# Optimization experiments

Measured on AMD Instinct MI355X. Metric: run time of the kernel, lower is better.

Reference implementation:

```python
import jax, jax.numpy as jnp
import numpy as np

N_PATCHES = 14
PS = 16            # patch size: 224 / 14
C, H_IMG, W_IMG = 3, 224, 224
HIDDEN = 768
HEADS = 12
DH = HIDDEN // HEADS
BLOCKS = 12
MLP = 4 * HIDDEN
OUT = 1000
SEQ = N_PATCHES ** 2 + 1  # 197
BATCH = 64


def get_positional_embeddings(seq_len, d):
    # sin(i/10000^(j/d)) for even j, cos(i/10000^((j-1)/d)) for odd j
    i = jnp.arange(seq_len, dtype=jnp.float32)[:, None]
    j = jnp.arange(d)[None, :]
    even = (j % 2 == 0)
    expo = jnp.where(even, j, j - 1).astype(jnp.float32) / d
    ang = i / (10000.0 ** expo)
    return jnp.where(even, jnp.sin(ang), jnp.cos(ang))


def layernorm(x, g, b, eps=1e-5):
    mu = x.mean(-1, keepdims=True)
    var = ((x - mu) ** 2).mean(-1, keepdims=True)
    return (x - mu) / jnp.sqrt(var + eps) * g + b


def mhsa(x, qw, qb, kw, kb, vw, vb):
    # x: [B,S,HIDDEN]; per-head linears qw/kw/vw: [H,DH,DH] (torch Linear weight layout)
    B, S, _ = x.shape
    xh = x.reshape(B, S, HEADS, DH)
    q = jnp.einsum('bshd,hed->bshe', xh, qw) + qb
    k = jnp.einsum('bshd,hed->bshe', xh, kw) + kb
    v = jnp.einsum('bshd,hed->bshe', xh, vw) + vb
    scores = jnp.einsum('bshe,bthe->bhst', q, k) / jnp.sqrt(jnp.float32(DH))
    attn = jax.nn.softmax(scores, axis=-1)
    out = jnp.einsum('bhst,bthe->bshe', attn, v)
    return out.reshape(B, S, HIDDEN)


def vit_block(x, p):
    ln1_g, ln1_b, qw, qb, kw, kb, vw, vb, ln2_g, ln2_b, w1, b1, w2, b2 = p
    x = x + mhsa(layernorm(x, ln1_g, ln1_b), qw, qb, kw, kb, vw, vb)
    h = layernorm(x, ln2_g, ln2_b)
    h = jax.nn.gelu(h @ w1.T + b1, approximate=False) @ w2.T + b2
    return x + h


def patchify(images):
    # [N,C,H,W] -> [N, n_patches^2, C*PS*PS], channel-major within each patch
    n = images.shape[0]
    x = images.reshape(n, C, N_PATCHES, PS, N_PATCHES, PS)
    x = x.transpose(0, 2, 4, 1, 3, 5)  # n, pi, pj, c, ps, ps
    return x.reshape(n, N_PATCHES * N_PATCHES, C * PS * PS)


def setup_inputs() -> dict:
    key = jax.random.key(0)
    ks = jax.random.split(key, 20)
    s = 0.02
    return {
        'images': jax.random.normal(ks[0], (BATCH, C, H_IMG, W_IMG), jnp.float32),
        'mapper_w': jax.random.normal(ks[1], (HIDDEN, C * PS * PS), jnp.float32) * s,
        'mapper_b': jnp.zeros((HIDDEN,), jnp.float32),
        'cls_token': jax.random.uniform(ks[2], (1, HIDDEN), jnp.float32),
        'ln1_g': jnp.ones((BLOCKS, HIDDEN), jnp.float32),
        'ln1_b': jnp.zeros((BLOCKS, HIDDEN), jnp.float32),
        'qw': jax.random.normal(ks[3], (BLOCKS, HEADS, DH, DH), jnp.float32) * s,
        'qb': jnp.zeros((BLOCKS, HEADS, DH), jnp.float32),
        'kw': jax.random.normal(ks[4], (BLOCKS, HEADS, DH, DH), jnp.float32) * s,
        'kb': jnp.zeros((BLOCKS, HEADS, DH), jnp.float32),
        'vw': jax.random.normal(ks[5], (BLOCKS, HEADS, DH, DH), jnp.float32) * s,
        'vb': jnp.zeros((BLOCKS, HEADS, DH), jnp.float32),
        'ln2_g': jnp.ones((BLOCKS, HIDDEN), jnp.float32),
        'ln2_b': jnp.zeros((BLOCKS, HIDDEN), jnp.float32),
        'w1': jax.random.normal(ks[6], (BLOCKS, MLP, HIDDEN), jnp.float32) * s,
        'b1': jnp.zeros((BLOCKS, MLP), jnp.float32),
        'w2': jax.random.normal(ks[7], (BLOCKS, HIDDEN, MLP), jnp.float32) * s,
        'b2': jnp.zeros((BLOCKS, HIDDEN), jnp.float32),
        'head_w': jax.random.normal(ks[8], (OUT, HIDDEN), jnp.float32) * s,
        'head_b': jnp.zeros((OUT,), jnp.float32),
    }


def reference(images, mapper_w, mapper_b, cls_token, ln1_g, ln1_b, qw, qb, kw, kb,
              vw, vb, ln2_g, ln2_b, w1, b1, w2, b2, head_w, head_b):
    n = images.shape[0]
    patches = patchify(images)
    tokens = patches @ mapper_w.T + mapper_b                      # [B, 196, HIDDEN]
    cls = jnp.broadcast_to(cls_token[None], (n, 1, HIDDEN))
    tokens = jnp.concatenate([cls, tokens], axis=1)               # [B, 197, HIDDEN]
    out = tokens + get_positional_embeddings(SEQ, HIDDEN)[None]

    stacked = (ln1_g, ln1_b, qw, qb, kw, kb, vw, vb, ln2_g, ln2_b, w1, b1, w2, b2)

    def step(x, p):
        return vit_block(x, p), None

    out, _ = jax.lax.scan(step, out, stacked)
    cls_out = out[:, 0]                                           # [B, HIDDEN]
    return jax.nn.softmax(cls_out @ head_w.T + head_b, axis=-1)
```

## Files before the change

kernel.cpp:

```cpp
#include <hip/hip_runtime.h>
#include <cstdint>
#include <cstddef>
#include <cstdio>

using u16 = unsigned short;
using u32 = unsigned int;

typedef __attribute__((ext_vector_type(8))) __bf16 bf16x8;
typedef __attribute__((ext_vector_type(4))) float f32x4;

struct alignas(16) U128 { u32 w[4]; };
struct alignas(16) F4   { float x[4]; };
struct alignas(8)  US4  { u16 h[4]; };

#define DEVFN static __device__ __forceinline__

DEVFN u16 f2bf(float x) {
  union { float f; u32 u; } v; v.f = x;
  u32 r = v.u + 0x7fffu + ((v.u >> 16) & 1u);
  return (u16)(r >> 16);
}

DEVFN bf16x8 ld16(const u16* p) { return __builtin_bit_cast(bf16x8, *(const U128*)p); }

DEVFN f32x4 mfma16(bf16x8 a, bf16x8 b, f32x4 c) {
  return __builtin_amdgcn_mfma_f32_16x16x32_bf16(a, b, c, 0, 0, 0);
}

DEVFN void gload_lds16(const u16* g, u16* l) {
  __builtin_amdgcn_global_load_lds(
      (const __attribute__((address_space(1))) void*)g,
      (__attribute__((address_space(3))) void*)l, 16, 0, 0);
}

DEVFN float gelu(float x) {
  float z = fabsf(x) * 0.70710678118f;
  float t = __builtin_amdgcn_rcpf(1.f + 0.3275911f * z);
  float p = t * (0.254829592f + t * (-0.284496736f + t * (1.421413741f +
            t * (-1.453152027f + t * 1.061405429f))));
  float e = __expf(-z * z);
  float erfz = 1.f - p * e;
  erfz = copysignf(erfz, x);
  return 0.5f * x * (1.f + erfz);
}

DEVFN void remap_bid(int bid, int Mb, int Nb, int& bm, int& bn) {
  const int ngrp  = Mb >> 3;
  const int per   = Nb << 3;
  const int nfull = ngrp * per;
  if (bid < nfull) {
    const int bmg = bid / per;
    const int rem = bid - bmg * per;
    bn = rem >> 3;
    bm = (bmg << 3) + (rem & 7);
  } else {
    const int r = bid - nfull;
    const int q = r / Nb;
    bm = (ngrp << 3) + q;
    bn = r - q * Nb;
  }
}

constexpr int SEQL   = 197;
constexpr int NB     = 64;
constexpr int NH     = 12;
constexpr int MROWS  = NB * SEQL;
constexpr int MPAD   = 12672;
constexpr int MPAD2  = 12800;
constexpr int MPATCH = NB * 196;
constexpr int SP     = 208;
constexpr int SP2    = 224;
constexpr int BHN    = NB * NH;

constexpr size_t OFF_X    = 0;
constexpr size_t OFF_ALN  = OFF_X    + (size_t)MPAD * 768 * 4;
constexpr size_t OFF_H    = OFF_ALN  + (size_t)MPAD2 * 768 * 2;
constexpr size_t OFF_WQKV = OFF_H    + (size_t)MPAD2 * 3072 * 2;
constexpr size_t OFF_W1   = OFF_WQKV + (size_t)2304 * 128 * 2;
constexpr size_t OFF_W2   = OFF_W1   + (size_t)3072 * 768 * 2;
constexpr size_t OFF_WMAP = OFF_W2   + (size_t)3072 * 768 * 2;
constexpr size_t OFF_Q    = OFF_WMAP + (size_t)768 * 768 * 2;
constexpr size_t OFF_K    = OFF_Q    + (size_t)BHN * SP * 64 * 2;
constexpr size_t OFF_VT   = OFF_K    + (size_t)BHN * SP * 64 * 2;
constexpr size_t OFF_PAT  = OFF_VT   + (size_t)BHN * 64 * SP2 * 2;
constexpr size_t OFF_POS  = OFF_PAT  + (size_t)MPATCH * 768 * 2;
constexpr size_t WS_NEED  = OFF_POS  + (size_t)SEQL * 768 * 4;

__global__ void zero_kernel(u32* __restrict__ p, long n) {
  long i = (long)blockIdx.x * 256 + threadIdx.x;
  long stride = (long)gridDim.x * 256;
  for (; i < n; i += stride) p[i] = 0u;
}

__global__ void cvt_kernel(const float* __restrict__ src, u16* __restrict__ dst, int n) {
  int i = blockIdx.x * 256 + threadIdx.x;
  if (i < n) dst[i] = f2bf(src[i]);
}

__global__ void pos_kernel(float* __restrict__ pos) {
  int i = blockIdx.x * 256 + threadIdx.x;
  if (i >= SEQL * 768) return;
  int s = i / 768, j = i - s * 768;
  float expo = (float)(j & ~1) * (1.0f / 768.0f);
  float ang  = (float)s * expf(-expo * logf(10000.0f));
  pos[i] = (j & 1) ? cosf(ang) : sinf(ang);
}

__global__ void cls_kernel(const float* __restrict__ cls, const float* __restrict__ pos,
                           float* __restrict__ X) {
  int b = blockIdx.x;
  for (int c = threadIdx.x; c < 768; c += 256)
    X[(size_t)b * SEQL * 768 + c] = cls[c] + pos[c];
}

__global__ void patchify_kernel(const float* __restrict__ img, u16* __restrict__ out) {
  int i = blockIdx.x * 256 + threadIdx.x;
  if (i >= MPATCH * 768) return;
  int m = i / 768, k = i - m * 768;
  int b = m / 196, p = m - b * 196;
  int py = p / 14, px = p - py * 14;
  int c = k >> 8, rem = k & 255, iy = rem >> 4, ix = rem & 15;
  float v = img[(((size_t)b * 3 + c) * 224 + py * 16 + iy) * 224 + px * 16 + ix];
  out[i] = f2bf(v);
}

__global__ void prep_kernel(const float* __restrict__ qw, const float* __restrict__ kw,
                            const float* __restrict__ vw, const float* __restrict__ w1,
                            const float* __restrict__ w2,
                            u16* __restrict__ Wqkv, u16* __restrict__ W1b,
                            u16* __restrict__ W2b, int blk) {
  const int NQ = 2304 * 128;
  const int NV = 3072 * 768 / 4;
  int i = blockIdx.x * 256 + threadIdx.x;
  if (i < NQ) {
    int n = i >> 7, kk = i & 127;
    int p = n / 768, ef = n - p * 768;
    int h = ef >> 6, e = ef & 63;
    float v = 0.f;
    if ((kk >> 6) == (h & 1)) {
      int d = kk & 63;
      const float* w = (p == 0) ? qw : (p == 1) ? kw : vw;
      v = w[(((size_t)blk * NH + h) * 64 + e) * 64 + d];
    }
    Wqkv[i] = f2bf(v);
  } else if (i < NQ + NV) {
    int j = (i - NQ) * 4;
    F4 v = *(const F4*)(w1 + (size_t)blk * 3072 * 768 + j);
    US4 o;
    #pragma unroll
    for (int r = 0; r < 4; ++r) o.h[r] = f2bf(v.x[r]);
    *(US4*)(W1b + j) = o;
  } else if (i < NQ + 2 * NV) {
    int j = (i - NQ - NV) * 4;
    F4 v = *(const F4*)(w2 + (size_t)blk * 3072 * 768 + j);
    US4 o;
    #pragma unroll
    for (int r = 0; r < 4; ++r) o.h[r] = f2bf(v.x[r]);
    *(US4*)(W2b + j) = o;
  }
}

__global__ __launch_bounds__(256) void ln_kernel(const float* __restrict__ X,
    const float* __restrict__ g, const float* __restrict__ b, u16* __restrict__ out) {
  int row  = blockIdx.x * 4 + (threadIdx.x >> 6);
  int lane = threadIdx.x & 63;
  const float* x = X + (size_t)row * 768 + lane * 12;
  F4 a0 = *(const F4*)(x);
  F4 a1 = *(const F4*)(x + 4);
  F4 a2 = *(const F4*)(x + 8);
  float v[12];
  #pragma unroll
  for (int j = 0; j < 4; ++j) { v[j] = a0.x[j]; v[4 + j] = a1.x[j]; v[8 + j] = a2.x[j]; }
  float s = 0.f, q = 0.f;
  #pragma unroll
  for (int j = 0; j < 12; ++j) { s += v[j]; q += v[j] * v[j]; }
  #pragma unroll
  for (int d = 1; d < 64; d <<= 1) { s += __shfl_xor(s, d); q += __shfl_xor(q, d); }
  float mu  = s * (1.f / 768.f);
  float var = q * (1.f / 768.f) - mu * mu;
  float rs  = rsqrtf(var + 1e-5f);
  const float* gp = g + lane * 12;
  const float* bp = b + lane * 12;
  u16* op = out + (size_t)row * 768 + lane * 12;
  u16 o[12];
  #pragma unroll
  for (int j = 0; j < 12; ++j) o[j] = f2bf((v[j] - mu) * rs * gp[j] + bp[j]);
  #pragma unroll
  for (int c = 0; c < 3; ++c) {
    US4 w; w.h[0] = o[c*4]; w.h[1] = o[c*4+1]; w.h[2] = o[c*4+2]; w.h[3] = o[c*4+3];
    *(US4*)(op + c * 4) = w;
  }
}

enum { EPI_PATCH = 0, EPI_QKV = 1, EPI_GELU = 2, EPI_RESID = 3 };

template<int EPI>
__global__ __launch_bounds__(256, 3) void gemm128(
    const u16* __restrict__ A, const u16* __restrict__ B, int K, int lda, int ldb,
    int Mb, int Nb,
    const float* __restrict__ e0, const float* __restrict__ e1, const float* __restrict__ e2,
    float* __restrict__ f0, const float* __restrict__ f1,
    u16* __restrict__ o0, u16* __restrict__ o1, u16* __restrict__ o2) {
  __shared__ u16 Ab[3][128 * 32];
  __shared__ u16 Bb[3][128 * 32];
  const int tid  = threadIdx.x;
  const int wave = tid >> 6, lane = tid & 63;
  int bm, bn;
  remap_bid(blockIdx.x, Mb, Nb, bm, bn);
  const int fr = lane & 15, fg = lane >> 4;
  const int srow = wave * 16 + (lane >> 2);
  const int gcol = ((lane & 3) ^ ((lane >> 3) & 3)) * 8;
  const u16* gA = A + (size_t)(bm * 128 + srow) * lda + gcol;
  const u16* gB = B + (size_t)(bn * 128 + srow) * ldb + gcol;
  const int wm = (wave >> 1) * 64, wn = (wave & 1) * 64;
  const int sl = (fg ^ ((fr >> 1) & 3)) * 8;
  const int nt = K >> 5;

  auto STAGE = [&](int c, int t) {
    gload_lds16(gA + t * 32,                    &Ab[c][0] + wave * 512);
    gload_lds16(gA + t * 32 + (size_t)64 * lda, &Ab[c][0] + wave * 512 + 2048);
    gload_lds16(gB + t * 32,                    &Bb[c][0] + wave * 512);
    gload_lds16(gB + t * 32 + (size_t)64 * ldb, &Bb[c][0] + wave * 512 + 2048);
  };

  f32x4 acc[4][4] = {};
  STAGE(0, 0);
  if (nt > 1) STAGE(1, 1);
  int bi = 0;
  for (int t = 0; t < nt; ++t) {
    if (t + 1 < nt) asm volatile("s_waitcnt vmcnt(4)" ::: "memory");
    else            asm volatile("s_waitcnt vmcnt(0)" ::: "memory");
    __builtin_amdgcn_s_barrier();
    if (t + 2 < nt) { int si = bi + 2; if (si >= 3) si -= 3; STAGE(si, t + 2); }
    const u16* ab   = &Ab[bi][0];
    const u16* bbuf = &Bb[bi][0];
    bf16x8 af[4], bfv[4];
    #pragma unroll
    for (int i = 0; i < 4; ++i) af[i]  = ld16(ab + (wm + i * 16 + fr) * 32 + sl);
    #pragma unroll
    for (int j = 0; j < 4; ++j) bfv[j] = ld16(bbuf + (wn + j * 16 + fr) * 32 + sl);
    __builtin_amdgcn_s_setprio(1);
    #pragma unroll
    for (int i = 0; i < 4; ++i)
      #pragma unroll
      for (int j = 0; j < 4; ++j)
        acc[i][j] = mfma16(af[i], bfv[j], acc[i][j]);
    __builtin_amdgcn_s_setprio(0);
    bi = (bi + 1 == 3) ? 0 : bi + 1;
  }

  #pragma unroll
  for (int i = 0; i < 4; ++i) {
    #pragma unroll
    for (int r = 0; r < 4; ++r) {
      const int m = bm * 128 + wm + i * 16 + fg * 4 + r;
      if constexpr (EPI == EPI_PATCH) {
        const int bb = m / 196;
        const int s  = m - bb * 196 + 1;
        float* xrow = f0 + ((size_t)bb * SEQL + s) * 768;
        const float* prow = f1 + (size_t)s * 768;
        #pragma unroll
        for (int j = 0; j < 4; ++j) {
          const int n = bn * 128 + wn + j * 16 + fr;
          xrow[n] = acc[i][j][r] + e0[n] + prow[n];
        }
      } else if constexpr (EPI == EPI_GELU) {
        u16* hrow = o0 + (size_t)m * 3072;
        #pragma unroll
        for (int j = 0; j < 4; ++j) {
          const int n = bn * 128 + wn + j * 16 + fr;
          hrow[n] = f2bf(gelu(acc[i][j][r] + e0[n]));
        }
      } else {
        if (m < MROWS) {
          float* xrow = f0 + (size_t)m * 768;
          #pragma unroll
          for (int j = 0; j < 4; ++j) {
            const int n = bn * 128 + wn + j * 16 + fr;
            xrow[n] += acc[i][j][r] + e0[n];
          }
        }
      }
    }
  }
}

__global__ __launch_bounds__(256, 2) void qkv_gemm(
    const u16* __restrict__ A, const u16* __restrict__ B,
    const float* __restrict__ e0, const float* __restrict__ e1, const float* __restrict__ e2,
    u16* __restrict__ o0, u16* __restrict__ o1, u16* __restrict__ o2) {
  __shared__ u16 Ab[4][128 * 32];
  __shared__ u16 Bb[4][128 * 32];
  const int tid = threadIdx.x, wave = tid >> 6, lane = tid & 63;
  int bm, bn;
  remap_bid(blockIdx.x, MPAD / 128, 18, bm, bn);
  const int fr = lane & 15, fg = lane >> 4;
  const u16* Aw = A + (bn % 6) * 128;
  const int srow = wave * 16 + (lane >> 2);
  const int gcol = ((lane & 3) ^ ((lane >> 3) & 3)) * 8;
  const u16* gA = Aw + (size_t)(bm * 128 + srow) * 768 + gcol;
  const u16* gB = B + (size_t)(bn * 128 + srow) * 128 + gcol;
  const int wm = (wave >> 1) * 64, wn = (wave & 1) * 64;
  const int sl = (fg ^ ((fr >> 1) & 3)) * 8;

  #pragma unroll
  for (int c = 0; c < 4; ++c) {
    gload_lds16(gA + c * 32,                    &Ab[c][0] + wave * 512);
    gload_lds16(gA + c * 32 + (size_t)64 * 768, &Ab[c][0] + wave * 512 + 2048);
    gload_lds16(gB + c * 32,                    &Bb[c][0] + wave * 512);
    gload_lds16(gB + c * 32 + (size_t)64 * 128, &Bb[c][0] + wave * 512 + 2048);
  }
  asm volatile("s_waitcnt vmcnt(0)" ::: "memory");
  __builtin_amdgcn_s_barrier();

  f32x4 acc[4][4] = {};
  #pragma unroll
  for (int c = 0; c < 4; ++c) {
    bf16x8 af[4], bfv[4];
    #pragma unroll
    for (int i = 0; i < 4; ++i) af[i]  = ld16(&Ab[c][0] + (wm + i * 16 + fr) * 32 + sl);
    #pragma unroll
    for (int j = 0; j < 4; ++j) bfv[j] = ld16(&Bb[c][0] + (wn + j * 16 + fr) * 32 + sl);
    __builtin_amdgcn_s_setprio(1);
    #pragma unroll
    for (int i = 0; i < 4; ++i)
      #pragma unroll
      for (int j = 0; j < 4; ++j)
        acc[i][j] = mfma16(af[i], bfv[j], acc[i][j]);
    __builtin_amdgcn_s_setprio(0);
  }

  #pragma unroll
  for (int i = 0; i < 4; ++i) {
    #pragma unroll
    for (int r = 0; r < 4; ++r) {
      const int m = bm * 128 + wm + i * 16 + fg * 4 + r;
      if (m < MROWS) {
        const int bb = m / 197;
        const int s  = m - bb * 197;
        #pragma unroll
        for (int j = 0; j < 4; ++j) {
          const int n = bn * 128 + wn + j * 16 + fr;
          const int p = n / 768;
          const int ef = n - p * 768;
          const int h = ef >> 6, e = ef & 63;
          const size_t bh = (size_t)bb * NH + h;
          if (p == 0)      o0[(bh * SP + s) * 64 + e] = f2bf((acc[i][j][r] + e0[ef]) * 0.125f);
          else if (p == 1) o1[(bh * SP + s) * 64 + e] = f2bf(acc[i][j][r] + e1[ef]);
          else             o2[(bh * 64 + e) * SP2 + s] = f2bf(acc[i][j][r] + e2[ef]);
        }
      }
    }
  }
}

__global__ __launch_bounds__(256, 2) void attn_kernel(const u16* __restrict__ Q,
    const u16* __restrict__ Km, const u16* __restrict__ Vt, float* __restrict__ X) {
  __shared__ u16  P[4][16 * SP2];
  __shared__ u16  Kl[208 * 72];
  __shared__ float sums[4][16];
  const int bh = blockIdx.x;
  const int b = bh / NH, h = bh - b * NH;
  const int wave = threadIdx.x >> 6, lane = threadIdx.x & 63;
  const int fr = lane & 15, fg = lane >> 4;
  const u16* Qb = Q  + (size_t)bh * SP * 64;
  const u16* Kb = Km + (size_t)bh * SP * 64;
  const u16* Vb = Vt + (size_t)bh * 64 * SP2;
  {
    const int r0 = threadIdx.x >> 2;
    const int e  = (threadIdx.x & 3) * 16;
    #pragma unroll
    for (int rr = r0; rr < 208; rr += 64)
      *(U128*)(Kl + rr * 72 + e) = *(const U128*)(Kb + (size_t)rr * 64 + e);
  }
  __syncthreads();
  u16* Pl = &P[wave][0];
  for (int qt = wave; qt < 13; qt += 4) {
    const int s0 = qt * 16;
    bf16x8 qf0 = ld16(Qb + (size_t)(s0 + fr) * 64 + fg * 8);
    bf16x8 qf1 = ld16(Qb + (size_t)(s0 + fr) * 64 + 32 + fg * 8);
    f32x4 sc[13];
    #pragma unroll
    for (int tf = 0; tf < 13; ++tf) {
      f32x4 a = {0.f, 0.f, 0.f, 0.f};
      bf16x8 k0 = ld16(Kl + (tf * 16 + fr) * 72 + fg * 8);
      bf16x8 k1 = ld16(Kl + (tf * 16 + fr) * 72 + 32 + fg * 8);
      a = mfma16(qf0, k0, a);
      a = mfma16(qf1, k1, a);
      sc[tf] = a;
    }
    float mx[4] = {-3e38f, -3e38f, -3e38f, -3e38f};
    #pragma unroll
    for (int tf = 0; tf < 13; ++tf) {
      const bool ok = (tf * 16 + fr) < 197;
      #pragma unroll
      for (int r = 0; r < 4; ++r) {
        float v = ok ? sc[tf][r] : -3e38f;
        sc[tf][r] = v;
        mx[r] = fmaxf(mx[r], v);
      }
    }
    #pragma unroll
    for (int r = 0; r < 4; ++r)
      #pragma unroll
      for (int d = 1; d < 16; d <<= 1) mx[r] = fmaxf(mx[r], __shfl_xor(mx[r], d));
    float sm[4] = {0.f, 0.f, 0.f, 0.f};
    #pragma unroll
    for (int tf = 0; tf < 13; ++tf) {
      #pragma unroll
      for (int r = 0; r < 4; ++r) {
        float e = __expf(sc[tf][r] - mx[r]);
        sm[r] += e;
        Pl[(fg * 4 + r) * SP2 + tf * 16 + fr] = f2bf(e);
      }
    }
    #pragma unroll
    for (int r = 0; r < 4; ++r) {
      #pragma unroll
      for (int d = 1; d < 16; d <<= 1) sm[r] += __shfl_xor(sm[r], d);
      if (fr == 0) sums[wave][fg * 4 + r] = sm[r];
    }
    #pragma unroll
    for (int r = 0; r < 4; ++r) Pl[(fg * 4 + r) * SP2 + 208 + fr] = 0;
    f32x4 o[4] = {};
    #pragma unroll
    for (int ks = 0; ks < 7; ++ks) {
      bf16x8 pf = ld16(Pl + fr * SP2 + ks * 32 + fg * 8);
      #pragma unroll
      for (int ef = 0; ef < 4; ++ef) {
        bf16x8 vf = ld16(Vb + (size_t)(ef * 16 + fr) * SP2 + ks * 32 + fg * 8);
        o[ef] = mfma16(vf, pf, o[ef]);
      }
    }
    const float inv = 1.f / sums[wave][fr];
    const int s = s0 + fr;
    if (s < 197) {
      float* xp = X + ((size_t)b * SEQL + s) * 768 + h * 64;
      #pragma unroll
      for (int ef = 0; ef < 4; ++ef)
        #pragma unroll
        for (int r = 0; r < 4; ++r)
          xp[ef * 16 + fg * 4 + r] += o[ef][r] * inv;
    }
  }
}

__global__ __launch_bounds__(256) void head_kernel(const float* __restrict__ X,
    const float* __restrict__ hw, const float* __restrict__ hb, float* __restrict__ out) {
  __shared__ float xr[768];
  __shared__ float lg[1000];
  __shared__ float red[8];
  const int b = blockIdx.x, tid = threadIdx.x;
  for (int c = tid; c < 768; c += 256) xr[c] = X[(size_t)b * SEQL * 768 + c];
  __syncthreads();
  for (int n = tid; n < 1000; n += 256) {
    const F4* w4 = (const F4*)(hw + (size_t)n * 768);
    const F4* x4 = (const F4*)xr;
    float acc = hb[n];
    for (int k = 0; k < 192; ++k) {
      F4 w = w4[k]; F4 xv = x4[k];
      acc += w.x[0] * xv.x[0] + w.x[1] * xv.x[1] + w.x[2] * xv.x[2] + w.x[3] * xv.x[3];
    }
    lg[n] = acc;
  }
  __syncthreads();
  float m = -3e38f;
  for (int n = tid; n < 1000; n += 256) m = fmaxf(m, lg[n]);
  #pragma unroll
  for (int d = 1; d < 64; d <<= 1) m = fmaxf(m, __shfl_xor(m, d));
  if ((tid & 63) == 0) red[tid >> 6] = m;
  __syncthreads();
  m = fmaxf(fmaxf(red[0], red[1]), fmaxf(red[2], red[3]));
  float s = 0.f;
  for (int n = tid; n < 1000; n += 256) s += expf(lg[n] - m);
  #pragma unroll
  for (int d = 1; d < 64; d <<= 1) s += __shfl_xor(s, d);
  if ((tid & 63) == 0) red[4 + (tid >> 6)] = s;
  __syncthreads();
  s = red[4] + red[5] + red[6] + red[7];
  const float inv = 1.f / s;
  for (int n = tid; n < 1000; n += 256) out[(size_t)b * 1000 + n] = expf(lg[n] - m) * inv;
}

extern "C" void kernel_launch(void* const* d_in, const int* in_sizes, int n_in,
                              void* d_out, int out_size, void* d_ws, size_t ws_size,
                              hipStream_t stream) {
  (void)in_sizes; (void)n_in; (void)out_size;
  if (ws_size < WS_NEED) { printf("ws too small: %zu < %zu\n", ws_size, WS_NEED); return; }

  const float* images   = (const float*)d_in[0];
  const float* mapper_w = (const float*)d_in[1];
  const float* mapper_b = (const float*)d_in[2];
  const float* cls_tok  = (const float*)d_in[3];
  const float* ln1_g    = (const float*)d_in[4];
  const float* ln1_b    = (const float*)d_in[5];
  const float* qw       = (const float*)d_in[6];
  const float* qb       = (const float*)d_in[7];
  const float* kw       = (const float*)d_in[8];
  const float* kb       = (const float*)d_in[9];
  const float* vw       = (const float*)d_in[10];
  const float* vb       = (const float*)d_in[11];
  const float* ln2_g    = (const float*)d_in[12];
  const float* ln2_b    = (const float*)d_in[13];
  const float* w1       = (const float*)d_in[14];
  const float* b1       = (const float*)d_in[15];
  const float* w2       = (const float*)d_in[16];
  const float* b2       = (const float*)d_in[17];
  const float* head_w   = (const float*)d_in[18];
  const float* head_b   = (const float*)d_in[19];

  char* ws = (char*)d_ws;
  float* X    = (float*)(ws + OFF_X);
  u16*  Aln   = (u16*)(ws + OFF_ALN);
  u16*  Hb    = (u16*)(ws + OFF_H);
  u16*  Wqkv  = (u16*)(ws + OFF_WQKV);
  u16*  W1b   = (u16*)(ws + OFF_W1);
  u16*  W2b   = (u16*)(ws + OFF_W2);
  u16*  Wmap  = (u16*)(ws + OFF_WMAP);
  u16*  Qb    = (u16*)(ws + OFF_Q);
  u16*  Kb    = (u16*)(ws + OFF_K);
  u16*  Vtb   = (u16*)(ws + OFF_VT);
  u16*  Pat   = (u16*)(ws + OFF_PAT);
  float* Pos  = (float*)(ws + OFF_POS);

  zero_kernel<<<2048, 256, 0, stream>>>((u32*)Qb,  (long)(BHN * SP * 64 / 2));
  zero_kernel<<<2048, 256, 0, stream>>>((u32*)Kb,  (long)(BHN * SP * 64 / 2));
  zero_kernel<<<2048, 256, 0, stream>>>((u32*)Vtb, (long)(BHN * 64 * SP2 / 2));
  zero_kernel<<<64,   256, 0, stream>>>((u32*)(X + (size_t)MROWS * 768), (long)((MPAD - MROWS) * 768));

  pos_kernel<<<(SEQL * 768 + 255) / 256, 256, 0, stream>>>(Pos);
  cvt_kernel<<<(768 * 768 + 255) / 256, 256, 0, stream>>>(mapper_w, Wmap, 768 * 768);
  patchify_kernel<<<(MPATCH * 768 + 255) / 256, 256, 0, stream>>>(images, Pat);
  cls_kernel<<<NB, 256, 0, stream>>>(cls_tok, Pos, X);

  gemm128<EPI_PATCH><<<(MPATCH / 128) * (768 / 128), 256, 0, stream>>>(
      Pat, Wmap, 768, 768, 768, MPATCH / 128, 768 / 128,
      mapper_b, nullptr, nullptr, X, Pos, nullptr, nullptr, nullptr);

  const int PREP_N = 2304 * 128 + 2 * (3072 * 768 / 4);
  for (int blk = 0; blk < 12; ++blk) {
    ln_kernel<<<MPAD / 4, 256, 0, stream>>>(X, ln1_g + blk * 768, ln1_b + blk * 768, Aln);
    prep_kernel<<<(PREP_N + 255) / 256, 256, 0, stream>>>(
        qw, kw, vw, w1, w2, Wqkv, W1b, W2b, blk);
    qkv_gemm<<<(MPAD / 128) * 18, 256, 0, stream>>>(
        Aln, Wqkv, qb + blk * 768, kb + blk * 768, vb + blk * 768, Qb, Kb, Vtb);
    attn_kernel<<<BHN, 256, 0, stream>>>(Qb, Kb, Vtb, X);
    ln_kernel<<<MPAD / 4, 256, 0, stream>>>(X, ln2_g + blk * 768, ln2_b + blk * 768, Aln);
    gemm128<EPI_GELU><<<(MPAD / 128) * (3072 / 128), 256, 0, stream>>>(
        Aln, W1b, 768, 768, 768, MPAD / 128, 3072 / 128,
        b1 + blk * 3072, nullptr, nullptr, nullptr, nullptr, Hb, nullptr, nullptr);
    gemm128<EPI_RESID><<<(MPAD / 128) * (768 / 128), 256, 0, stream>>>(
        Hb, W2b, 3072, 3072, 3072, MPAD / 128, 768 / 128,
        b2 + blk * 768, nullptr, nullptr, X, nullptr, nullptr, nullptr, nullptr);
  }

  head_kernel<<<NB, 256, 0, stream>>>(X, head_w, head_b, (float*)d_out);
}
```

Measured before the change: 4.126 ms.

## Hoist weight conversion, zero only attention padding, persistent FC1 GELU GEMM

```diff
diff --git a/kernel.cpp b/kernel.cpp
--- a/kernel.cpp
+++ b/kernel.cpp
@@ -72,24 +72,45 @@
 constexpr int SP2    = 224;
 constexpr int BHN    = NB * NH;
 
+constexpr int QSZ    = 2304 * 128;
+constexpr int WSZ    = 3072 * 768;
+
 constexpr size_t OFF_X    = 0;
 constexpr size_t OFF_ALN  = OFF_X    + (size_t)MPAD * 768 * 4;
 constexpr size_t OFF_H    = OFF_ALN  + (size_t)MPAD2 * 768 * 2;
-constexpr size_t OFF_WQKV = OFF_H    + (size_t)MPAD2 * 3072 * 2;
-constexpr size_t OFF_W1   = OFF_WQKV + (size_t)2304 * 128 * 2;
-constexpr size_t OFF_W2   = OFF_W1   + (size_t)3072 * 768 * 2;
-constexpr size_t OFF_WMAP = OFF_W2   + (size_t)3072 * 768 * 2;
+constexpr size_t OFF_WMAP = OFF_H    + (size_t)MPAD2 * 3072 * 2;
 constexpr size_t OFF_Q    = OFF_WMAP + (size_t)768 * 768 * 2;
 constexpr size_t OFF_K    = OFF_Q    + (size_t)BHN * SP * 64 * 2;
 constexpr size_t OFF_VT   = OFF_K    + (size_t)BHN * SP * 64 * 2;
 constexpr size_t OFF_PAT  = OFF_VT   + (size_t)BHN * 64 * SP2 * 2;
 constexpr size_t OFF_POS  = OFF_PAT  + (size_t)MPATCH * 768 * 2;
-constexpr size_t WS_NEED  = OFF_POS  + (size_t)SEQL * 768 * 4;
+constexpr size_t OFF_WTS  = OFF_POS  + (size_t)SEQL * 768 * 4;
+constexpr size_t WS_SMALL = OFF_WTS + (size_t)(QSZ + 2 * WSZ) * 2;
+constexpr size_t WS_BIG   = OFF_WTS + (size_t)12 * (QSZ + 2 * WSZ) * 2;
 
 __global__ void zero_kernel(u32* __restrict__ p, long n) {
   long i = (long)blockIdx.x * 256 + threadIdx.x;
   long stride = (long)gridDim.x * 256;
   for (; i < n; i += stride) p[i] = 0u;
+}
+
+__global__ void padzero_kernel(u16* __restrict__ Q, u16* __restrict__ Kp,
+                               u16* __restrict__ Vt) {
+  const int NQ32 = BHN * 352;
+  const int NV   = BHN * 64 * 27;
+  int i = blockIdx.x * 256 + threadIdx.x;
+  if (i < NQ32) {
+    int bh = i / 352, r = i - bh * 352;
+    ((u32*)(Q + ((size_t)bh * SP + 197) * 64))[r] = 0u;
+  } else if (i < 2 * NQ32) {
+    int j = i - NQ32;
+    int bh = j / 352, r = j - bh * 352;
+    ((u32*)(Kp + ((size_t)bh * SP + 197) * 64))[r] = 0u;
+  } else if (i < 2 * NQ32 + NV) {
+    int j = i - 2 * NQ32;
+    int be = j / 27, s = j - be * 27;
+    Vt[(size_t)be * SP2 + 197 + s] = 0;
+  }
 }
 
 __global__ void cvt_kernel(const float* __restrict__ src, u16* __restrict__ dst, int n) {
@@ -124,15 +145,52 @@
   out[i] = f2bf(v);
 }
 
+__global__ void prep_all(const float* __restrict__ qw, const float* __restrict__ kw,
+                         const float* __restrict__ vw, const float* __restrict__ w1,
+                         const float* __restrict__ w2,
+                         u16* __restrict__ Wq, u16* __restrict__ W1b,
+                         u16* __restrict__ W2b) {
+  const int NQ = 12 * QSZ;
+  const int NV = 12 * (WSZ / 4);
+  int i = blockIdx.x * 256 + threadIdx.x;
+  if (i < NQ) {
+    int blk = i / QSZ;
+    int r = i - blk * QSZ;
+    int n = r >> 7, kk = r & 127;
+    int p = n / 768, ef = n - p * 768;
+    int h = ef >> 6, e = ef & 63;
+    float v = 0.f;
+    if ((kk >> 6) == (h & 1)) {
+      int d = kk & 63;
+      const float* w = (p == 0) ? qw : (p == 1) ? kw : vw;
+      v = w[(((size_t)blk * NH + h) * 64 + e) * 64 + d];
+    }
+    Wq[i] = f2bf(v);
+  } else if (i < NQ + NV) {
+    int j = (i - NQ) * 4;
+    F4 v = *(const F4*)(w1 + j);
+    US4 o;
+    #pragma unroll
+    for (int r = 0; r < 4; ++r) o.h[r] = f2bf(v.x[r]);
+    *(US4*)(W1b + j) = o;
+  } else if (i < NQ + 2 * NV) {
+    int j = (i - NQ - NV) * 4;
+    F4 v = *(const F4*)(w2 + j);
+    US4 o;
+    #pragma unroll
+    for (int r = 0; r < 4; ++r) o.h[r] = f2bf(v.x[r]);
+    *(US4*)(W2b + j) = o;
+  }
+}
+
 __global__ void prep_kernel(const float* __restrict__ qw, const float* __restrict__ kw,
                             const float* __restrict__ vw, const float* __restrict__ w1,
                             const float* __restrict__ w2,
                             u16* __restrict__ Wqkv, u16* __restrict__ W1b,
                             u16* __restrict__ W2b, int blk) {
-  const int NQ = 2304 * 128;
-  const int NV = 3072 * 768 / 4;
+  const int NV = WSZ / 4;
   int i = blockIdx.x * 256 + threadIdx.x;
-  if (i < NQ) {
+  if (i < QSZ) {
     int n = i >> 7, kk = i & 127;
     int p = n / 768, ef = n - p * 768;
     int h = ef >> 6, e = ef & 63;
@@ -143,16 +201,16 @@
       v = w[(((size_t)blk * NH + h) * 64 + e) * 64 + d];
     }
     Wqkv[i] = f2bf(v);
-  } else if (i < NQ + NV) {
-    int j = (i - NQ) * 4;
-    F4 v = *(const F4*)(w1 + (size_t)blk * 3072 * 768 + j);
+  } else if (i < QSZ + NV) {
+    int j = (i - QSZ) * 4;
+    F4 v = *(const F4*)(w1 + (size_t)blk * WSZ + j);
     US4 o;
     #pragma unroll
     for (int r = 0; r < 4; ++r) o.h[r] = f2bf(v.x[r]);
     *(US4*)(W1b + j) = o;
-  } else if (i < NQ + 2 * NV) {
-    int j = (i - NQ - NV) * 4;
-    F4 v = *(const F4*)(w2 + (size_t)blk * 3072 * 768 + j);
+  } else if (i < QSZ + 2 * NV) {
+    int j = (i - QSZ - NV) * 4;
+    F4 v = *(const F4*)(w2 + (size_t)blk * WSZ + j);
     US4 o;
     #pragma unroll
     for (int r = 0; r < 4; ++r) o.h[r] = f2bf(v.x[r]);
@@ -264,13 +322,6 @@
           const int n = bn * 128 + wn + j * 16 + fr;
           xrow[n] = acc[i][j][r] + e0[n] + prow[n];
         }
-      } else if constexpr (EPI == EPI_GELU) {
-        u16* hrow = o0 + (size_t)m * 3072;
-        #pragma unroll
-        for (int j = 0; j < 4; ++j) {
-          const int n = bn * 128 + wn + j * 16 + fr;
-          hrow[n] = f2bf(gelu(acc[i][j][r] + e0[n]));
-        }
       } else {
         if (m < MROWS) {
           float* xrow = f0 + (size_t)m * 768;
@@ -279,6 +330,89 @@
             const int n = bn * 128 + wn + j * 16 + fr;
             xrow[n] += acc[i][j][r] + e0[n];
           }
+        }
+      }
+    }
+  }
+}
+
+__global__ __launch_bounds__(256, 3) void gemm128f_gelu(
+    const u16* __restrict__ A, const u16* __restrict__ B,
+    const float* __restrict__ e0, u16* __restrict__ o0,
+    int ntiles, int nblocks) {
+  __shared__ u16 Ab[3][128 * 32];
+  __shared__ u16 Bb[3][128 * 32];
+  constexpr int lda = 768, ldb = 768, nt = 24;
+  const int tid = threadIdx.x, wave = tid >> 6, lane = tid & 63;
+  const int fr = lane & 15, fg = lane >> 4;
+  const int srow = wave * 16 + (lane >> 2);
+  const int gcol = ((lane & 3) ^ ((lane >> 3) & 3)) * 8;
+  const int wm = (wave >> 1) * 64, wn = (wave & 1) * 64;
+  const int sl = (fg ^ ((fr >> 1) & 3)) * 8;
+  const int myTiles = (ntiles - (int)blockIdx.x + nblocks - 1) / nblocks;
+  const int total = myTiles * nt;
+
+  int s_t  = blockIdx.x;
+  int s_kk = 0;
+  const u16 *s_gA, *s_gB;
+  {
+    int bm, bn; remap_bid(s_t, 99, 24, bm, bn);
+    s_gA = A + (size_t)(bm * 128 + srow) * lda + gcol;
+    s_gB = B + (size_t)(bn * 128 + srow) * ldb + gcol;
+  }
+  auto STAGE1 = [&](int c) {
+    gload_lds16(s_gA + s_kk * 32,                    &Ab[c][0] + wave * 512);
+    gload_lds16(s_gA + s_kk * 32 + (size_t)64 * lda, &Ab[c][0] + wave * 512 + 2048);
+    gload_lds16(s_gB + s_kk * 32,                    &Bb[c][0] + wave * 512);
+    gload_lds16(s_gB + s_kk * 32 + (size_t)64 * ldb, &Bb[c][0] + wave * 512 + 2048);
+    if (++s_kk == nt) {
+      s_kk = 0;
+      s_t += nblocks;
+      if (s_t < ntiles) {
+        int bm, bn; remap_bid(s_t, 99, 24, bm, bn);
+        s_gA = A + (size_t)(bm * 128 + srow) * lda + gcol;
+        s_gB = B + (size_t)(bn * 128 + srow) * ldb + gcol;
+      }
+    }
+  };
+
+  STAGE1(0);
+  if (total > 1) STAGE1(1);
+  int bi = 0, g = 0;
+  for (int t = blockIdx.x; t < ntiles; t += nblocks) {
+    int bm, bn; remap_bid(t, 99, 24, bm, bn);
+    f32x4 acc[4][4] = {};
+    for (int k = 0; k < nt; ++k, ++g) {
+      if (g + 1 < total) asm volatile("s_waitcnt vmcnt(4)" ::: "memory");
+      else               asm volatile("s_waitcnt vmcnt(0)" ::: "memory");
+      __builtin_amdgcn_s_barrier();
+      if (g + 2 < total) { int si = bi + 2; if (si >= 3) si -= 3; STAGE1(si); }
+      const u16* ab   = &Ab[bi][0];
+      const u16* bbuf = &Bb[bi][0];
+      bf16x8 af[4], bfv[4];
+      #pragma unroll
+      for (int i = 0; i < 4; ++i) af[i]  = ld16(ab + (wm + i * 16 + fr) * 32 + sl);
+      #pragma unroll
+      for (int j = 0; j < 4; ++j) bfv[j] = ld16(bbuf + (wn + j * 16 + fr) * 32 + sl);
+      __builtin_amdgcn_s_setprio(1);
+      #pragma unroll
+      for (int i = 0; i < 4; ++i)
+        #pragma unroll
+        for (int j = 0; j < 4; ++j)
+          acc[i][j] = mfma16(af[i], bfv[j], acc[i][j]);
+      __builtin_amdgcn_s_setprio(0);
+      bi = (bi + 1 == 3) ? 0 : bi + 1;
+    }
+    #pragma unroll
+    for (int i = 0; i < 4; ++i) {
+      #pragma unroll
+      for (int r = 0; r < 4; ++r) {
+        const int m = bm * 128 + wm + i * 16 + fg * 4 + r;
+        u16* hrow = o0 + (size_t)m * 3072;
+        #pragma unroll
+        for (int j = 0; j < 4; ++j) {
+          const int n = bn * 128 + wn + j * 16 + fr;
+          hrow[n] = f2bf(gelu(acc[i][j][r] + e0[n]));
         }
       }
     }
@@ -486,7 +620,8 @@
                               void* d_out, int out_size, void* d_ws, size_t ws_size,
                               hipStream_t stream) {
   (void)in_sizes; (void)n_in; (void)out_size;
-  if (ws_size < WS_NEED) { printf("ws too small: %zu < %zu\n", ws_size, WS_NEED); return; }
+  if (ws_size < WS_SMALL) { printf("ws too small: %zu < %zu\n", ws_size, WS_SMALL); return; }
+  const bool hoist = ws_size >= WS_BIG;
 
   const float* images   = (const float*)d_in[0];
   const float* mapper_w = (const float*)d_in[1];
@@ -513,44 +648,49 @@
   float* X    = (float*)(ws + OFF_X);
   u16*  Aln   = (u16*)(ws + OFF_ALN);
   u16*  Hb    = (u16*)(ws + OFF_H);
-  u16*  Wqkv  = (u16*)(ws + OFF_WQKV);
-  u16*  W1b   = (u16*)(ws + OFF_W1);
-  u16*  W2b   = (u16*)(ws + OFF_W2);
   u16*  Wmap  = (u16*)(ws + OFF_WMAP);
   u16*  Qb    = (u16*)(ws + OFF_Q);
   u16*  Kb    = (u16*)(ws + OFF_K);
   u16*  Vtb   = (u16*)(ws + OFF_VT);
   u16*  Pat   = (u16*)(ws + OFF_PAT);
   float* Pos  = (float*)(ws + OFF_POS);
-
-  zero_kernel<<<2048, 256, 0, stream>>>((u32*)Qb,  (long)(BHN * SP * 64 / 2));
-  zero_kernel<<<2048, 256, 0, stream>>>((u32*)Kb,  (long)(BHN * SP * 64 / 2));
-  zero_kernel<<<2048, 256, 0, stream>>>((u32*)Vtb, (long)(BHN * 64 * SP2 / 2));
-  zero_kernel<<<64,   256, 0, stream>>>((u32*)(X + (size_t)MROWS * 768), (long)((MPAD - MROWS) * 768));
+  u16*  WqA   = (u16*)(ws + OFF_WTS);
+  u16*  W1A   = WqA + (size_t)(hoist ? 12 : 1) * QSZ;
+  u16*  W2A   = W1A + (size_t)(hoist ? 12 : 1) * WSZ;
+
+  padzero_kernel<<<(2 * BHN * 352 + BHN * 64 * 27 + 255) / 256, 256, 0, stream>>>(Qb, Kb, Vtb);
+  zero_kernel<<<64, 256, 0, stream>>>((u32*)(X + (size_t)MROWS * 768), (long)((MPAD - MROWS) * 768));
 
   pos_kernel<<<(SEQL * 768 + 255) / 256, 256, 0, stream>>>(Pos);
   cvt_kernel<<<(768 * 768 + 255) / 256, 256, 0, stream>>>(mapper_w, Wmap, 768 * 768);
   patchify_kernel<<<(MPATCH * 768 + 255) / 256, 256, 0, stream>>>(images, Pat);
   cls_kernel<<<NB, 256, 0, stream>>>(cls_tok, Pos, X);
 
+  if (hoist) {
+    const int N_ALL = 12 * QSZ + 2 * 12 * (WSZ / 4);
+    prep_all<<<(N_ALL + 255) / 256, 256, 0, stream>>>(qw, kw, vw, w1, w2, WqA, W1A, W2A);
+  }
+
   gemm128<EPI_PATCH><<<(MPATCH / 128) * (768 / 128), 256, 0, stream>>>(
       Pat, Wmap, 768, 768, 768, MPATCH / 128, 768 / 128,
       mapper_b, nullptr, nullptr, X, Pos, nullptr, nullptr, nullptr);
 
-  const int PREP_N = 2304 * 128 + 2 * (3072 * 768 / 4);
+  const int PREP_N = QSZ + 2 * (WSZ / 4);
   for (int blk = 0; blk < 12; ++blk) {
+    u16* Wq_b = WqA + (size_t)(hoist ? blk : 0) * QSZ;
+    u16* W1_b = W1A + (size_t)(hoist ? blk : 0) * WSZ;
+    u16* W2_b = W2A + (size_t)(hoist ? blk : 0) * WSZ;
     ln_kernel<<<MPAD / 4, 256, 0, stream>>>(X, ln1_g + blk * 768, ln1_b + blk * 768, Aln);
-    prep_kernel<<<(PREP_N + 255) / 256, 256, 0, stream>>>(
-        qw, kw, vw, w1, w2, Wqkv, W1b, W2b, blk);
+    if (!hoist)
+      prep_kernel<<<(PREP_N + 255) / 256, 256, 0, stream>>>(
+          qw, kw, vw, w1, w2, Wq_b, W1_b, W2_b, blk);
     qkv_gemm<<<(MPAD / 128) * 18, 256, 0, stream>>>(
-        Aln, Wqkv, qb + blk * 768, kb + blk * 768, vb + blk * 768, Qb, Kb, Vtb);
+        Aln, Wq_b, qb + blk * 768, kb + blk * 768, vb + blk * 768, Qb, Kb, Vtb);
     attn_kernel<<<BHN, 256, 0, stream>>>(Qb, Kb, Vtb, X);
     ln_kernel<<<MPAD / 4, 256, 0, stream>>>(X, ln2_g + blk * 768, ln2_b + blk * 768, Aln);
-    gemm128<EPI_GELU><<<(MPAD / 128) * (3072 / 128), 256, 0, stream>>>(
-        Aln, W1b, 768, 768, 768, MPAD / 128, 3072 / 128,
-        b1 + blk * 3072, nullptr, nullptr, nullptr, nullptr, Hb, nullptr, nullptr);
+    gemm128f_gelu<<<768, 256, 0, stream>>>(Aln, W1_b, b1 + blk * 3072, Hb, 2376, 768);
     gemm128<EPI_RESID><<<(MPAD / 128) * (768 / 128), 256, 0, stream>>>(
-        Hb, W2b, 3072, 3072, 3072, MPAD / 128, 768 / 128,
+        Hb, W2_b, 3072, 3072, 3072, MPAD / 128, 768 / 128,
         b2 + blk * 768, nullptr, nullptr, X, nullptr, nullptr, nullptr, nullptr);
   }
 
```

New measurement: 4.107 ms. No clear change (-0.5%).
